# Optimization experiments

Measured on AMD Instinct MI355X. Metric: run time of the kernel, lower is better.

The kernel has to match this reference:

```python
import jax, jax.numpy as jnp
import numpy as np

B, S, D = 4, 2048, 1024
MULT = 4
INNER = MULT * D
E = 4          # n_expert
K = 1          # top-k
ALPHA = 0.5


def setup_inputs() -> dict:
    key = jax.random.key(0)
    ks = jax.random.split(key, 8)
    std = 0.02
    x = jax.random.normal(ks[0], (B, S, D), jnp.float32)
    W1 = jax.random.normal(ks[1], (D, INNER), jnp.float32) * std
    b1 = jnp.zeros((INNER,), jnp.float32)
    W2 = jax.random.normal(ks[2], (INNER, D), jnp.float32) * std
    b2 = jnp.zeros((D,), jnp.float32)
    Wg = jax.random.normal(ks[3], (D, E), jnp.float32) * std
    ew1 = jax.random.normal(ks[4], (E, D, INNER), jnp.float32) * std
    ew3 = jax.random.normal(ks[5], (E, D, INNER), jnp.float32) * std
    ew2 = jax.random.normal(ks[6], (E, INNER, D), jnp.float32) * std
    return {"x": x, "W1": W1, "b1": b1, "W2": W2, "b2": b2,
            "Wg": Wg, "ew1": ew1, "ew3": ew3, "ew2": ew2}


def reference(x, W1, b1, W2, b2, Wg, ew1, ew3, ew2):
    # Dense branch: Linear -> GELU (exact, torch default) -> Linear
    y_dense = jax.nn.gelu(x @ W1 + b1, approximate=False) @ W2 + b2

    # MoE branch: top-k softmax routing, SwiGLU experts
    logits = x @ Wg                                   # [B,S,E]
    probs = jax.nn.softmax(logits, axis=-1)
    topv, topi = jax.lax.top_k(probs, K)              # [B,S,K]
    gates = topv / jnp.sum(topv, axis=-1, keepdims=True)  # renormalize top-k
    onehot = jax.nn.one_hot(topi, E, dtype=x.dtype)   # [B,S,K,E]
    combine = jnp.sum(gates[..., None] * onehot, axis=-2)  # [B,S,E]

    y_moe = jnp.zeros_like(x)
    for e in range(E):  # small fixed expert count
        h = jax.nn.silu(x @ ew1[e]) * (x @ ew3[e])    # [B,S,INNER]
        y_moe = y_moe + combine[..., e:e + 1] * (h @ ew2[e])

    # Load-balancing aux loss: E * sum_e f_e * P_e
    frac = jnp.mean(jnp.sum(onehot, axis=-2), axis=(0, 1)) / K  # [E]
    pmean = jnp.mean(probs, axis=(0, 1))                        # [E]
    aux = E * jnp.sum(frac * pmean)

    y = ALPHA * y_dense + (1.0 - ALPHA) * y_moe
    return (y, aux)
```

## Files before the change

kernel.cpp:

```cpp
#include <hip/hip_runtime.h>
#include <hip/hip_bf16.h>


static constexpr int MT = 8192;
static constexpr int DD = 1024;
static constexpr int DI = 4096;

typedef float f32x4 __attribute__((ext_vector_type(4)));
typedef __bf16 bf16x8 __attribute__((ext_vector_type(8)));
typedef unsigned short u16;

__device__ __forceinline__ u16 f2bf(float f) {
    union { __hip_bfloat16 b; u16 u; } v;
    v.b = __float2bfloat16(f);
    return v.u;
}

__device__ __forceinline__ void gload_lds16(const void* g, void* l) {
    __builtin_amdgcn_global_load_lds(
        (const __attribute__((address_space(1))) void*)g,
        (__attribute__((address_space(3))) void*)l, 16, 0, 0);
}

__device__ __forceinline__ float gelu_f(float v) {
    return 0.5f * v * (1.0f + erff(v * 0.70710678118654752f));
}
__device__ __forceinline__ float silu_f(float v) {
    return v / (1.0f + expf(-v));
}

#define FENCE() asm volatile("" ::: "memory")
#define BARRIER() do { FENCE(); __builtin_amdgcn_s_barrier(); FENCE(); } while (0)
#define WAIT_LGKM0() asm volatile("s_waitcnt lgkmcnt(0)" ::: "memory")

__global__ void __launch_bounds__(256) transpose_cvt(
    const float* __restrict__ src, u16* __restrict__ dst, int K, int N,
    int pack, int packOff, size_t srcMatStride, size_t dstMatStride) {
    __shared__ u16 t[64][72];
    const float* s = src + (size_t)blockIdx.z * srcMatStride;
    u16* d = dst + (size_t)blockIdx.z * dstMatStride;
    int n0 = blockIdx.x * 64, k0 = blockIdx.y * 64;
    int tid = threadIdx.x;
    int c = tid & 15;
    int r = tid >> 4;
#pragma unroll
    for (int p = 0; p < 4; ++p) {
        int k = r + p * 16;
        float4 v = *(const float4*)(s + (size_t)(k0 + k) * N + n0 + c * 4);
        t[c * 4 + 0][k] = f2bf(v.x);
        t[c * 4 + 1][k] = f2bf(v.y);
        t[c * 4 + 2][k] = f2bf(v.z);
        t[c * 4 + 3][k] = f2bf(v.w);
    }
    __syncthreads();
    int n = tid >> 2, kc = (tid & 3) * 16;
    const uint4* p0 = (const uint4*)&t[n][kc];
    uint4 a = p0[0], b = p0[1];
    int gn = n0 + n;
    int dr = pack ? ((gn >> 5) * 64 + (gn & 31) + packOff) : gn;
    uint4* o = (uint4*)(d + (size_t)dr * K + k0 + kc);
    o[0] = a; o[1] = b;
}

__global__ void __launch_bounds__(256) gate_kernel(
    const float* __restrict__ x, const float* __restrict__ Wg,
    float* __restrict__ psum_blk, int* __restrict__ expertA) {
    int w = threadIdx.x >> 6, l = threadIdx.x & 63;
    int t = blockIdx.x * 4 + w;
    const float* xr = x + (size_t)t * DD;
    double a0 = 0, a1 = 0, a2 = 0, a3 = 0;
#pragma unroll
    for (int i = 0; i < 4; ++i) {
        int k = i * 256 + l * 4;
        float4 xv = *(const float4*)(xr + k);
        float4 w0 = *(const float4*)(Wg + (size_t)(k + 0) * 4);
        float4 w1 = *(const float4*)(Wg + (size_t)(k + 1) * 4);
        float4 w2 = *(const float4*)(Wg + (size_t)(k + 2) * 4);
        float4 w3 = *(const float4*)(Wg + (size_t)(k + 3) * 4);
        a0 += (double)xv.x * w0.x + (double)xv.y * w1.x + (double)xv.z * w2.x + (double)xv.w * w3.x;
        a1 += (double)xv.x * w0.y + (double)xv.y * w1.y + (double)xv.z * w2.y + (double)xv.w * w3.y;
        a2 += (double)xv.x * w0.z + (double)xv.y * w1.z + (double)xv.z * w2.z + (double)xv.w * w3.z;
        a3 += (double)xv.x * w0.w + (double)xv.y * w1.w + (double)xv.z * w2.w + (double)xv.w * w3.w;
    }
#pragma unroll
    for (int o = 32; o; o >>= 1) {
        a0 += __shfl_down(a0, o); a1 += __shfl_down(a1, o);
        a2 += __shfl_down(a2, o); a3 += __shfl_down(a3, o);
    }
    __shared__ float wps[4][4];
    if (l == 0) {
        double lg[4] = {a0, a1, a2, a3};
        int best = 0;
#pragma unroll
        for (int e = 1; e < 4; ++e) if (lg[e] > lg[best]) best = e;
        double m = lg[best], s = 0, p[4];
#pragma unroll
        for (int e = 0; e < 4; ++e) { p[e] = exp(lg[e] - m); s += p[e]; }
#pragma unroll
        for (int e = 0; e < 4; ++e) wps[w][e] = (float)(p[e] / s);
        expertA[t] = best;
    }
    __syncthreads();
    if (threadIdx.x < 4)
        psum_blk[blockIdx.x * 4 + threadIdx.x] =
            wps[0][threadIdx.x] + wps[1][threadIdx.x] + wps[2][threadIdx.x] + wps[3][threadIdx.x];
}

__global__ void __launch_bounds__(1024) build_lists(
    const int* __restrict__ expertA, const float* __restrict__ psum_blk,
    int* __restrict__ dstArr, int* __restrict__ rev,
    int* __restrict__ offsets, float* __restrict__ auxOut) {
    __shared__ int sc[4][1024];
    __shared__ float fs[1024];
    __shared__ float psum_s[4];
    __shared__ int tot_s[4], off_s[4];
    int tid = threadIdx.x;
    int le[8]; int c[4] = {0, 0, 0, 0};
#pragma unroll
    for (int i = 0; i < 8; ++i) { int e = expertA[tid * 8 + i]; le[i] = e; c[e]++; }
#pragma unroll
    for (int e = 0; e < 4; ++e) sc[e][tid] = c[e];
    __syncthreads();
    for (int o = 1; o < 1024; o <<= 1) {
        int v[4];
#pragma unroll
        for (int e = 0; e < 4; ++e) v[e] = (tid >= o) ? sc[e][tid - o] : 0;
        __syncthreads();
#pragma unroll
        for (int e = 0; e < 4; ++e) if (tid >= o) sc[e][tid] += v[e];
        __syncthreads();
    }
    if (tid == 0) {
        int o = 0;
#pragma unroll
        for (int e = 0; e < 4; ++e) {
            tot_s[e] = sc[e][1023]; off_s[e] = o; offsets[e] = o; o += tot_s[e];
        }
        offsets[4] = o;
    }
    __syncthreads();
    int base[4];
#pragma unroll
    for (int e = 0; e < 4; ++e) base[e] = off_s[e] + sc[e][tid] - c[e];
#pragma unroll
    for (int i = 0; i < 8; ++i) {
        int e = le[i]; int d = base[e]++; int t = tid * 8 + i;
        dstArr[t] = d; rev[d] = t;
    }
    float ps[4];
#pragma unroll
    for (int e = 0; e < 4; ++e)
        ps[e] = psum_blk[(2 * tid) * 4 + e] + psum_blk[(2 * tid + 1) * 4 + e];
    for (int e = 0; e < 4; ++e) {
        fs[tid] = ps[e]; __syncthreads();
        for (int o = 512; o; o >>= 1) { if (tid < o) fs[tid] += fs[tid + o]; __syncthreads(); }
        if (tid == 0) psum_s[e] = fs[0];
        __syncthreads();
    }
    if (tid == 0) {
        float a = 0;
#pragma unroll
        for (int e = 0; e < 4; ++e)
            a += ((float)tot_s[e] * (1.f / 8192.f)) * (psum_s[e] * (1.f / 8192.f));
        auxOut[0] = 4.f * a;
    }
}

__global__ void __launch_bounds__(256) gather_kernel(
    const float* __restrict__ x, const int* __restrict__ dstArr,
    u16* __restrict__ xg) {
    int w = threadIdx.x >> 6, l = threadIdx.x & 63;
    int t = blockIdx.x * 4 + w;
    int dst = dstArr[t];
    const float* xr = x + (size_t)t * DD;
#pragma unroll
    for (int i = 0; i < 4; ++i) {
        int k = i * 256 + l * 4;
        float4 v = *(const float4*)(xr + k);
        ushort4 u;
        u.x = f2bf(v.x); u.y = f2bf(v.y); u.z = f2bf(v.z); u.w = f2bf(v.w);
        *(ushort4*)(xg + (size_t)dst * DD + k) = u;
    }
}

template <int MODE, int NF>
__global__ void __launch_bounds__(512, 2) gemm8(
    const u16* __restrict__ A, const u16* __restrict__ Bw,
    const float* __restrict__ bias,
    u16* __restrict__ outB, float* __restrict__ outF,
    const int* __restrict__ offsets, const int* __restrict__ rev,
    int N, int K) {
    constexpr int BN   = NF * 64;
    constexpr int WCW  = NF * 16;
    constexpr int AELT = 2 * 256 * 32;
    constexpr int BUFE = AELT + 2 * BN * 32;
    constexpr int NIB  = NF / 2;
    __shared__ u16 lds[2 * BUFE];

    const int tid = threadIdx.x;
    const int w = tid >> 6, l = tid & 63;
    const int lr = l & 15, lg = l >> 4;
    const int wr = w >> 2, wc = w & 3;

    int rowBase, rowsValid = 256;
    const u16* Bp = Bw;
    if constexpr (MODE >= 2) {
        int e = blockIdx.z;
        int off = offsets[e], cnt = offsets[e + 1] - off;
        if ((int)blockIdx.y * 256 >= cnt) return;
        rowBase = off + blockIdx.y * 256;
        rowsValid = cnt - (int)blockIdx.y * 256;
        if (rowsValid > 256) rowsValid = 256;
        Bp = Bw + (size_t)e * ((size_t)2 * DD * DI);
    } else {
        rowBase = blockIdx.y * 256;
    }
    const int colBase = blockIdx.x * BN;
    const int NT = K >> 6;

    auto stageA = [&](int kt, int b, int ks) {
        const int kk = (kt << 6) + (ks << 5);
#pragma unroll
        for (int i = 0; i < 2; ++i) {
            int o = ((w << 1) + i) * 512 + (l << 3);
            int o2 = o ^ (((o >> 8) & 1) << 4);
            gload_lds16(A + (size_t)(rowBase + (o2 >> 5)) * K + kk + (o2 & 31),
                        &lds[b * BUFE + ks * 8192 + ((w << 1) + i) * 512]);
        }
    };
    auto stageB = [&](int kt, int b, int ks) {
        const int kk = (kt << 6) + (ks << 5);
#pragma unroll
        for (int i = 0; i < NIB; ++i) {
            int o = (w * NIB + i) * 512 + (l << 3);
            int o2 = o ^ (((o >> 8) & 1) << 4);
            gload_lds16(Bp + (size_t)(colBase + (o2 >> 5)) * K + kk + (o2 & 31),
                        &lds[b * BUFE + AELT + ks * (BN * 32) + (w * NIB + i) * 512]);
        }
    };

#define WAIT_VMB() do { \
    if constexpr (NF == 4) asm volatile("s_waitcnt vmcnt(4)" ::: "memory"); \
    else                   asm volatile("s_waitcnt vmcnt(3)" ::: "memory"); \
} while (0)

#define READBF(b_, ks_) do { \
    _Pragma("unroll") \
    for (int n = 0; n < NF; ++n) { \
        int e_ = (wc * WCW + n * 16 + lr) * 32 + lg * 8; \
        e_ ^= ((e_ >> 8) & 1) << 4; \
        bf[n] = *(const bf16x8*)&lds[(b_) * BUFE + AELT + (ks_) * (BN * 32) + e_]; \
    } \
} while (0)

#define READAF(b_, ks_, mq_) do { \
    _Pragma("unroll") \
    for (int m = 0; m < 4; ++m) { \
        int e_ = (wr * 128 + ((mq_) * 4 + m) * 16 + lr) * 32 + lg * 8; \
        e_ ^= ((e_ >> 8) & 1) << 4; \
        af[m] = *(const bf16x8*)&lds[(b_) * BUFE + (ks_) * 8192 + e_]; \
    } \
} while (0)

#define DOMFMA(mq_) do { \
    __builtin_amdgcn_s_setprio(1); \
    _Pragma("unroll") \
    for (int m = 0; m < 4; ++m) \
    _Pragma("unroll") \
    for (int n = 0; n < NF; ++n) \
        acc[(mq_) * 4 + m][n] = __builtin_amdgcn_mfma_f32_16x16x32_bf16( \
            bf[n], af[m], acc[(mq_) * 4 + m][n], 0, 0, 0); \
    __builtin_amdgcn_s_setprio(0); \
} while (0)

    f32x4 acc[8][NF];
#pragma unroll
    for (int m = 0; m < 8; ++m)
#pragma unroll
        for (int n = 0; n < NF; ++n) acc[m][n] = (f32x4){0.f, 0.f, 0.f, 0.f};
    bf16x8 af[4], bf[NF];

    stageA(0, 0, 0); stageB(0, 0, 0); stageA(0, 0, 1); stageB(0, 0, 1);
    stageA(1, 1, 0); stageB(1, 1, 0);
    WAIT_VMB();
    BARRIER();

    for (int t = 0; t < NT; ++t) {
        const int cb = t & 1, nb = cb ^ 1;
        const int tp1 = (t + 1 < NT) ? t + 1 : NT - 1;
        const int tp2 = (t + 2 < NT) ? t + 2 : NT - 1;
        READBF(cb, 0); READAF(cb, 0, 0); stageA(tp1, nb, 1);
        BARRIER(); WAIT_LGKM0(); DOMFMA(0); BARRIER();
        READAF(cb, 0, 1); stageB(tp1, nb, 1);
        BARRIER(); WAIT_LGKM0(); DOMFMA(1); BARRIER();
        READBF(cb, 1); READAF(cb, 1, 0); stageA(tp2, cb, 0);
        BARRIER(); WAIT_LGKM0(); DOMFMA(0); BARRIER();
        READAF(cb, 1, 1); stageB(tp2, cb, 0);
        BARRIER(); WAIT_LGKM0(); DOMFMA(1);
        WAIT_VMB();
        BARRIER();
    }

#pragma unroll
    for (int m = 0; m < 8; ++m) {
        int rloc = wr * 128 + m * 16 + lr;
        if (MODE >= 2 && rloc >= rowsValid) continue;
        size_t grow = (size_t)(rowBase + rloc);
        if constexpr (MODE == 2) {
#pragma unroll
            for (int n = 0; n < 2; ++n) {
                int col = (colBase >> 1) + wc * 32 + n * 16 + lg * 4;
                f32x4 v1 = acc[m][n], v3 = acc[m][n + 2];
                ushort4 u;
                u.x = f2bf(silu_f(v1[0]) * v3[0]);
                u.y = f2bf(silu_f(v1[1]) * v3[1]);
                u.z = f2bf(silu_f(v1[2]) * v3[2]);
                u.w = f2bf(silu_f(v1[3]) * v3[3]);
                *(ushort4*)(outB + grow * N + col) = u;
            }
        } else {
#pragma unroll
            for (int n = 0; n < NF; ++n) {
                int col = colBase + wc * WCW + n * 16 + lg * 4;
                f32x4 v = acc[m][n];
                f32x4 bb = *(const f32x4*)(bias + col);
                ushort4 u;
                u.x = f2bf(gelu_f(v[0] + bb[0]));
                u.y = f2bf(gelu_f(v[1] + bb[1]));
                u.z = f2bf(gelu_f(v[2] + bb[2]));
                u.w = f2bf(gelu_f(v[3] + bb[3]));
                *(ushort4*)(outB + grow * N + col) = u;
            }
        }
    }
#undef WAIT_VMB
#undef READBF
#undef READAF
#undef DOMFMA
}

template <int DM>
__global__ void __launch_bounds__(256) gemm97(
    const u16* __restrict__ A, const u16* __restrict__ Bw,
    const float* __restrict__ bias, float* __restrict__ outF,
    const int* __restrict__ offsets, const int* __restrict__ rev,
    int N, int K) {
    __shared__ u16 ldsA[128 * 32];
    __shared__ u16 ldsB[128 * 32];
    int tid = threadIdx.x, w = tid >> 6, l = tid & 63;
    int wr = w >> 1, wc = w & 1;
    int rowBase, rowsValid = 128;
    const u16* Bp = Bw;
    if constexpr (DM == 1) {
        int e = blockIdx.z;
        int off = offsets[e], cnt = offsets[e + 1] - off;
        if ((int)blockIdx.y * 128 >= cnt) return;
        rowBase = off + blockIdx.y * 128;
        rowsValid = cnt - (int)blockIdx.y * 128;
        if (rowsValid > 128) rowsValid = 128;
        Bp = Bw + (size_t)e * DD * DI;
    } else {
        rowBase = blockIdx.y * 128;
    }
    int colBase = blockIdx.x * 128;

    f32x4 acc[4][4];
#pragma unroll
    for (int m = 0; m < 4; ++m)
#pragma unroll
        for (int n = 0; n < 4; ++n) acc[m][n] = (f32x4){0.f, 0.f, 0.f, 0.f};

    int lr = l & 15, lg = l >> 4;
    int ar = l >> 2, ac = (l & 3) * 8;

    const int nkt = K >> 5;
    for (int kt = 0; kt < nkt; ++kt) {
        int k0 = kt << 5;
        const u16* ga = A + (size_t)(rowBase + w * 32 + ar) * K + k0 + ac;
        gload_lds16(ga, &ldsA[(w * 32) * 32]);
        gload_lds16(ga + (size_t)16 * K, &ldsA[(w * 32 + 16) * 32]);
        const u16* gb = Bp + (size_t)(colBase + w * 32 + ar) * K + k0 + ac;
        gload_lds16(gb, &ldsB[(w * 32) * 32]);
        gload_lds16(gb + (size_t)16 * K, &ldsB[(w * 32 + 16) * 32]);
        __syncthreads();
        bf16x8 af[4], bfr[4];
#pragma unroll
        for (int m = 0; m < 4; ++m)
            af[m] = *(const bf16x8*)&ldsA[(wr * 64 + m * 16 + lr) * 32 + lg * 8];
#pragma unroll
        for (int n = 0; n < 4; ++n)
            bfr[n] = *(const bf16x8*)&ldsB[(wc * 64 + n * 16 + lr) * 32 + lg * 8];
#pragma unroll
        for (int m = 0; m < 4; ++m)
#pragma unroll
            for (int n = 0; n < 4; ++n)
                acc[m][n] = __builtin_amdgcn_mfma_f32_16x16x32_bf16(
                    bfr[n], af[m], acc[m][n], 0, 0, 0);
        __syncthreads();
    }

#pragma unroll
    for (int m = 0; m < 4; ++m) {
        int rloc = wr * 64 + m * 16 + lr;
        if (DM == 1 && rloc >= rowsValid) continue;
        int tok = rev[rowBase + rloc];
#pragma unroll
        for (int n = 0; n < 4; ++n) {
            int col = colBase + wc * 64 + n * 16 + lg * 4;
            f32x4 v = acc[m][n];
            if constexpr (DM == 0) {
                f32x4 bb = *(const f32x4*)(bias + col);
                f32x4 r;
#pragma unroll
                for (int j = 0; j < 4; ++j) r[j] = 0.5f * (v[j] + bb[j]);
                *(f32x4*)(outF + (size_t)tok * N + col) = r;
            } else {
                f32x4* p = (f32x4*)(outF + (size_t)tok * N + col);
                f32x4 o = *p;
#pragma unroll
                for (int j = 0; j < 4; ++j) o[j] += 0.5f * v[j];
                *p = o;
            }
        }
    }
}

extern "C" void kernel_launch(void* const* d_in, const int* in_sizes, int n_in,
                              void* d_out, int out_size, void* d_ws, size_t ws_size,
                              hipStream_t stream) {
    const float* x   = (const float*)d_in[0];
    const float* W1  = (const float*)d_in[1];
    const float* b1  = (const float*)d_in[2];
    const float* W2  = (const float*)d_in[3];
    const float* b2  = (const float*)d_in[4];
    const float* Wg  = (const float*)d_in[5];
    const float* ew1 = (const float*)d_in[6];
    const float* ew3 = (const float*)d_in[7];
    const float* ew2 = (const float*)d_in[8];
    float* y = (float*)d_out;
    float* auxOut = y + (size_t)MT * DD;

    char* ws = (char*)d_ws;
    size_t off = 0;
    auto take = [&](size_t b) -> void* {
        void* p = ws + off;
        off += (b + 255) & ~(size_t)255;
        return p;
    };
    u16* W1t   = (u16*)take((size_t)DI * DD * 2);
    u16* W2t   = (u16*)take((size_t)DI * DD * 2);
    u16* ew13t = (u16*)take((size_t)4 * 2 * DI * DD * 2);
    u16* ew2t  = (u16*)take((size_t)4 * DI * DD * 2);
    u16* xg    = (u16*)take((size_t)(MT + 256) * DD * 2);
    u16* hd    = (u16*)take((size_t)(MT + 256) * DI * 2);
    int* expertA  = (int*)take(MT * 4);
    int* dstArr   = (int*)take(MT * 4);
    int* revA     = (int*)take(MT * 4);
    float* psum_blk = (float*)take(2048 * 4 * 4);
    int* offsets  = (int*)take(64);
    u16* hg = hd;

    if (ws_size < off) return;

    dim3 blk(256);
    transpose_cvt<<<dim3(64, 16, 1), blk, 0, stream>>>(W1,  W1t,  DD, DI, 0, 0,  (size_t)DD * DI, (size_t)DD * DI);
    transpose_cvt<<<dim3(64, 16, 4), blk, 0, stream>>>(ew1, ew13t, DD, DI, 1, 0,  (size_t)DD * DI, (size_t)2 * DD * DI);
    transpose_cvt<<<dim3(64, 16, 4), blk, 0, stream>>>(ew3, ew13t, DD, DI, 1, 32, (size_t)DD * DI, (size_t)2 * DD * DI);
    transpose_cvt<<<dim3(16, 64, 1), blk, 0, stream>>>(W2,  W2t,  DI, DD, 0, 0,  (size_t)DD * DI, (size_t)DD * DI);
    transpose_cvt<<<dim3(16, 64, 4), blk, 0, stream>>>(ew2, ew2t, DI, DD, 0, 0,  (size_t)DD * DI, (size_t)DD * DI);
    gate_kernel<<<2048, 256, 0, stream>>>(x, Wg, psum_blk, expertA);
    build_lists<<<1, 1024, 0, stream>>>(expertA, psum_blk, dstArr, revA, offsets, auxOut);
    gather_kernel<<<2048, 256, 0, stream>>>(x, dstArr, xg);
    gemm8<0, 4><<<dim3(DI / 256, MT / 256), dim3(512), 0, stream>>>(
        xg, W1t, b1, hd, nullptr, nullptr, nullptr, DI, DD);
    gemm97<0><<<dim3(DD / 128, MT / 128), blk, 0, stream>>>(
        hd, W2t, b2, y, nullptr, revA, DD, DI);
    gemm8<2, 4><<<dim3(2 * DI / 256, MT / 256, 4), dim3(512), 0, stream>>>(
        xg, ew13t, nullptr, hg, nullptr, offsets, nullptr, DI, DD);
    gemm97<1><<<dim3(DD / 128, MT / 128, 4), blk, 0, stream>>>(
        hg, ew2t, nullptr, y, offsets, revA, DD, DI);
}
```

Before: 632.0 us.

## Fuse dense and expert down-projections into one K-concatenated GEMM, merge transposes

The dense W2 GEMM and the per-expert ew2 GEMM become one kernel. For each expert's rows it accumulates hd·W2 and then hg·ew2 into the same registers and writes y once. This removes the read-modify-write of y and one launch, and the weight-conversion launches drop from five to two. To free memory, the hd buffer now aliases ew13t, so the expert up-projection runs before the dense one. The dense rows are now read through the expert-sorted order. The dense rows are also split across the four expert grids, which could hurt load balance.

```diff
diff --git a/kernel.cpp b/kernel.cpp
--- a/kernel.cpp
+++ b/kernel.cpp
@@ -33,12 +33,10 @@
 #define BARRIER() do { FENCE(); __builtin_amdgcn_s_barrier(); FENCE(); } while (0)
 #define WAIT_LGKM0() asm volatile("s_waitcnt lgkmcnt(0)" ::: "memory")
 
-__global__ void __launch_bounds__(256) transpose_cvt(
-    const float* __restrict__ src, u16* __restrict__ dst, int K, int N,
-    int pack, int packOff, size_t srcMatStride, size_t dstMatStride) {
+__device__ __forceinline__ void transpose_tile(
+    const float* __restrict__ s, u16* __restrict__ d, int K, int N,
+    int pack, int packOff) {
     __shared__ u16 t[64][72];
-    const float* s = src + (size_t)blockIdx.z * srcMatStride;
-    u16* d = dst + (size_t)blockIdx.z * dstMatStride;
     int n0 = blockIdx.x * 64, k0 = blockIdx.y * 64;
     int tid = threadIdx.x;
     int c = tid & 15;
@@ -60,6 +58,34 @@
     int dr = pack ? ((gn >> 5) * 64 + (gn & 31) + packOff) : gn;
     uint4* o = (uint4*)(d + (size_t)dr * K + k0 + kc);
     o[0] = a; o[1] = b;
+}
+
+__global__ void __launch_bounds__(256) transpose_up(
+    const float* __restrict__ W1, const float* __restrict__ ew1,
+    const float* __restrict__ ew3, u16* __restrict__ W1t,
+    u16* __restrict__ ew13t) {
+    int z = blockIdx.z;
+    if (z == 0) {
+        transpose_tile(W1, W1t, DD, DI, 0, 0);
+    } else if (z <= 4) {
+        transpose_tile(ew1 + (size_t)(z - 1) * DD * DI,
+                       ew13t + (size_t)(z - 1) * 2 * DD * DI, DD, DI, 1, 0);
+    } else {
+        transpose_tile(ew3 + (size_t)(z - 5) * DD * DI,
+                       ew13t + (size_t)(z - 5) * 2 * DD * DI, DD, DI, 1, 32);
+    }
+}
+
+__global__ void __launch_bounds__(256) transpose_dn(
+    const float* __restrict__ W2, const float* __restrict__ ew2,
+    u16* __restrict__ W2t, u16* __restrict__ ew2t) {
+    int z = blockIdx.z;
+    if (z == 0) {
+        transpose_tile(W2, W2t, DI, DD, 0, 0);
+    } else {
+        transpose_tile(ew2 + (size_t)(z - 1) * DI * DD,
+                       ew2t + (size_t)(z - 1) * DI * DD, DI, DD, 0, 0);
+    }
 }
 
 __global__ void __launch_bounds__(256) gate_kernel(
@@ -339,29 +365,21 @@
 #undef DOMFMA
 }
 
-template <int DM>
-__global__ void __launch_bounds__(256) gemm97(
-    const u16* __restrict__ A, const u16* __restrict__ Bw,
-    const float* __restrict__ bias, float* __restrict__ outF,
-    const int* __restrict__ offsets, const int* __restrict__ rev,
-    int N, int K) {
+__global__ void __launch_bounds__(256) gemm97cat(
+    const u16* __restrict__ Ad, const u16* __restrict__ Ag,
+    const u16* __restrict__ W2t, const u16* __restrict__ ew2t,
+    const float* __restrict__ b2, float* __restrict__ y,
+    const int* __restrict__ offsets, const int* __restrict__ rev) {
     __shared__ u16 ldsA[128 * 32];
     __shared__ u16 ldsB[128 * 32];
     int tid = threadIdx.x, w = tid >> 6, l = tid & 63;
     int wr = w >> 1, wc = w & 1;
-    int rowBase, rowsValid = 128;
-    const u16* Bp = Bw;
-    if constexpr (DM == 1) {
-        int e = blockIdx.z;
-        int off = offsets[e], cnt = offsets[e + 1] - off;
-        if ((int)blockIdx.y * 128 >= cnt) return;
-        rowBase = off + blockIdx.y * 128;
-        rowsValid = cnt - (int)blockIdx.y * 128;
-        if (rowsValid > 128) rowsValid = 128;
-        Bp = Bw + (size_t)e * DD * DI;
-    } else {
-        rowBase = blockIdx.y * 128;
-    }
+    int e = blockIdx.z;
+    int off = offsets[e], cnt = offsets[e + 1] - off;
+    if ((int)blockIdx.y * 128 >= cnt) return;
+    int rowBase = off + blockIdx.y * 128;
+    int rowsValid = cnt - (int)blockIdx.y * 128;
+    if (rowsValid > 128) rowsValid = 128;
     int colBase = blockIdx.x * 128;
 
     f32x4 acc[4][4];
@@ -373,54 +391,52 @@
     int lr = l & 15, lg = l >> 4;
     int ar = l >> 2, ac = (l & 3) * 8;
 
-    const int nkt = K >> 5;
-    for (int kt = 0; kt < nkt; ++kt) {
-        int k0 = kt << 5;
-        const u16* ga = A + (size_t)(rowBase + w * 32 + ar) * K + k0 + ac;
-        gload_lds16(ga, &ldsA[(w * 32) * 32]);
-        gload_lds16(ga + (size_t)16 * K, &ldsA[(w * 32 + 16) * 32]);
-        const u16* gb = Bp + (size_t)(colBase + w * 32 + ar) * K + k0 + ac;
-        gload_lds16(gb, &ldsB[(w * 32) * 32]);
-        gload_lds16(gb + (size_t)16 * K, &ldsB[(w * 32 + 16) * 32]);
-        __syncthreads();
-        bf16x8 af[4], bfr[4];
-#pragma unroll
-        for (int m = 0; m < 4; ++m)
-            af[m] = *(const bf16x8*)&ldsA[(wr * 64 + m * 16 + lr) * 32 + lg * 8];
-#pragma unroll
-        for (int n = 0; n < 4; ++n)
-            bfr[n] = *(const bf16x8*)&ldsB[(wc * 64 + n * 16 + lr) * 32 + lg * 8];
-#pragma unroll
-        for (int m = 0; m < 4; ++m)
+    const u16* Bm = ew2t + (size_t)e * DD * DI;
+#pragma unroll 1
+    for (int half = 0; half < 2; ++half) {
+        const u16* Ap = half ? Ag : Ad;
+        const u16* Bp = half ? Bm : W2t;
+#pragma unroll 1
+        for (int kt = 0; kt < DI / 32; ++kt) {
+            int k0 = kt << 5;
+            const u16* ga = Ap + (size_t)(rowBase + w * 32 + ar) * DI + k0 + ac;
+            gload_lds16(ga, &ldsA[(w * 32) * 32]);
+            gload_lds16(ga + (size_t)16 * DI, &ldsA[(w * 32 + 16) * 32]);
+            const u16* gb = Bp + (size_t)(colBase + w * 32 + ar) * DI + k0 + ac;
+            gload_lds16(gb, &ldsB[(w * 32) * 32]);
+            gload_lds16(gb + (size_t)16 * DI, &ldsB[(w * 32 + 16) * 32]);
+            __syncthreads();
+            bf16x8 af[4], bfr[4];
+#pragma unroll
+            for (int m = 0; m < 4; ++m)
+                af[m] = *(const bf16x8*)&ldsA[(wr * 64 + m * 16 + lr) * 32 + lg * 8];
 #pragma unroll
             for (int n = 0; n < 4; ++n)
-                acc[m][n] = __builtin_amdgcn_mfma_f32_16x16x32_bf16(
-                    bfr[n], af[m], acc[m][n], 0, 0, 0);
-        __syncthreads();
+                bfr[n] = *(const bf16x8*)&ldsB[(wc * 64 + n * 16 + lr) * 32 + lg * 8];
+#pragma unroll
+            for (int m = 0; m < 4; ++m)
+#pragma unroll
+                for (int n = 0; n < 4; ++n)
+                    acc[m][n] = __builtin_amdgcn_mfma_f32_16x16x32_bf16(
+                        bfr[n], af[m], acc[m][n], 0, 0, 0);
+            __syncthreads();
+        }
     }
 
 #pragma unroll
     for (int m = 0; m < 4; ++m) {
         int rloc = wr * 64 + m * 16 + lr;
-        if (DM == 1 && rloc >= rowsValid) continue;
+        if (rloc >= rowsValid) continue;
         int tok = rev[rowBase + rloc];
 #pragma unroll
         for (int n = 0; n < 4; ++n) {
             int col = colBase + wc * 64 + n * 16 + lg * 4;
             f32x4 v = acc[m][n];
-            if constexpr (DM == 0) {
-                f32x4 bb = *(const f32x4*)(bias + col);
-                f32x4 r;
-#pragma unroll
-                for (int j = 0; j < 4; ++j) r[j] = 0.5f * (v[j] + bb[j]);
-                *(f32x4*)(outF + (size_t)tok * N + col) = r;
-            } else {
-                f32x4* p = (f32x4*)(outF + (size_t)tok * N + col);
-                f32x4 o = *p;
-#pragma unroll
-                for (int j = 0; j < 4; ++j) o[j] += 0.5f * v[j];
-                *p = o;
-            }
+            f32x4 bb = *(const f32x4*)(b2 + col);
+            f32x4 r;
+#pragma unroll
+            for (int j = 0; j < 4; ++j) r[j] = 0.5f * (v[j] + bb[j]);
+            *(f32x4*)(y + (size_t)tok * DD + col) = r;
         }
     }
 }
@@ -449,34 +465,31 @@
     };
     u16* W1t   = (u16*)take((size_t)DI * DD * 2);
     u16* W2t   = (u16*)take((size_t)DI * DD * 2);
-    u16* ew13t = (u16*)take((size_t)4 * 2 * DI * DD * 2);
     u16* ew2t  = (u16*)take((size_t)4 * DI * DD * 2);
     u16* xg    = (u16*)take((size_t)(MT + 256) * DD * 2);
-    u16* hd    = (u16*)take((size_t)(MT + 256) * DI * 2);
+    u16* hg    = (u16*)take((size_t)(MT + 256) * DI * 2);
     int* expertA  = (int*)take(MT * 4);
     int* dstArr   = (int*)take(MT * 4);
     int* revA     = (int*)take(MT * 4);
     float* psum_blk = (float*)take(2048 * 4 * 4);
     int* offsets  = (int*)take(64);
-    u16* hg = hd;
+    size_t ew13Bytes = (size_t)4 * 2 * DI * DD * 2;
+    size_t hdBytes   = (size_t)(MT + 256) * DI * 2;
+    u16* ew13t = (u16*)take(ew13Bytes > hdBytes ? ew13Bytes : hdBytes);
+    u16* hd    = ew13t;
 
     if (ws_size < off) return;
 
     dim3 blk(256);
-    transpose_cvt<<<dim3(64, 16, 1), blk, 0, stream>>>(W1,  W1t,  DD, DI, 0, 0,  (size_t)DD * DI, (size_t)DD * DI);
-    transpose_cvt<<<dim3(64, 16, 4), blk, 0, stream>>>(ew1, ew13t, DD, DI, 1, 0,  (size_t)DD * DI, (size_t)2 * DD * DI);
-    transpose_cvt<<<dim3(64, 16, 4), blk, 0, stream>>>(ew3, ew13t, DD, DI, 1, 32, (size_t)DD * DI, (size_t)2 * DD * DI);
-    transpose_cvt<<<dim3(16, 64, 1), blk, 0, stream>>>(W2,  W2t,  DI, DD, 0, 0,  (size_t)DD * DI, (size_t)DD * DI);
-    transpose_cvt<<<dim3(16, 64, 4), blk, 0, stream>>>(ew2, ew2t, DI, DD, 0, 0,  (size_t)DD * DI, (size_t)DD * DI);
+    transpose_up<<<dim3(DI / 64, DD / 64, 9), blk, 0, stream>>>(W1, ew1, ew3, W1t, ew13t);
+    transpose_dn<<<dim3(DD / 64, DI / 64, 5), blk, 0, stream>>>(W2, ew2, W2t, ew2t);
     gate_kernel<<<2048, 256, 0, stream>>>(x, Wg, psum_blk, expertA);
     build_lists<<<1, 1024, 0, stream>>>(expertA, psum_blk, dstArr, revA, offsets, auxOut);
     gather_kernel<<<2048, 256, 0, stream>>>(x, dstArr, xg);
+    gemm8<2, 4><<<dim3(2 * DI / 256, MT / 256, 4), dim3(512), 0, stream>>>(
+        xg, ew13t, nullptr, hg, nullptr, offsets, nullptr, DI, DD);
     gemm8<0, 4><<<dim3(DI / 256, MT / 256), dim3(512), 0, stream>>>(
         xg, W1t, b1, hd, nullptr, nullptr, nullptr, DI, DD);
-    gemm97<0><<<dim3(DD / 128, MT / 128), blk, 0, stream>>>(
-        hd, W2t, b2, y, nullptr, revA, DD, DI);
-    gemm8<2, 4><<<dim3(2 * DI / 256, MT / 256, 4), dim3(512), 0, stream>>>(
-        xg, ew13t, nullptr, hg, nullptr, offsets, nullptr, DI, DD);
-    gemm97<1><<<dim3(DD / 128, MT / 128, 4), blk, 0, stream>>>(
-        hg, ew2t, nullptr, y, offsets, revA, DD, DI);
-}
+    gemm97cat<<<dim3(DD / 128, MT / 128, 4), blk, 0, stream>>>(
+        hd, hg, W2t, ew2t, b2, y, offsets, revA);
+}
```

Result: faster. 604.1 us (-4.4%).
